# Performance work log

Hardware: AMD Instinct MI355X
Metric: run time of the kernel (lower is better)

Reference implementation:

```python
import jax, jax.numpy as jnp
import numpy as np

B, S, H = 64, 4096, 256
NEG = 1e30


def setup_inputs() -> dict:
    key = jax.random.key(0)
    k1, k2, k3, k4, k5 = jax.random.split(key, 5)
    inp_seq = jax.random.normal(k1, (B, S, H), dtype=jnp.float32)
    mask = jax.random.randint(k2, (B, S), 0, 2).astype(jnp.float32)
    mask = mask.at[:, 0].set(1.0)  # ensure at least one valid position per row
    query = jax.random.normal(k3, (B, H), dtype=jnp.float32)
    # nn.Linear(2H, H): weight [H, 2H], bias [H]
    lim = 1.0 / np.sqrt(2 * H)
    W = jax.random.uniform(k4, (H, 2 * H), minval=-lim, maxval=lim, dtype=jnp.float32)
    b = jax.random.uniform(k5, (H,), minval=-lim, maxval=lim, dtype=jnp.float32)
    return {"inp_seq": inp_seq, "mask": mask, "query": query, "W": W, "b": b}


def reference(inp_seq, mask, query, W, b):
    # single-query attention pooling
    score = jnp.einsum("bsh,bh->bs", inp_seq, query)          # [B,S]
    score = score - NEG * (1.0 - mask)                          # additive mask
    att = jax.nn.softmax(score, axis=-1)                        # [B,S]
    extracted_msg = jnp.einsum("bs,bsh->bh", att, inp_seq)     # [B,H]
    conc = jnp.concatenate([query, extracted_msg], axis=1)      # [B,2H]
    control_emb = conc @ W.T + b                                # [B,H]
    return (extracted_msg, control_emb)
```

## Files before the change

### kernel.cpp

```cpp
#include <hip/hip_runtime.h>
#include <math.h>

namespace {
constexpr int kB = 64;
constexpr int kS = 4096;
constexpr int kH = 256;
constexpr int kChunks = 32;
constexpr int kChunkS = kS / kChunks;
constexpr int kWavesPerBlock = 4;
constexpr int kPosPerWave = kChunkS / kWavesPerBlock;
constexpr int kPartStride = kH + 2;
constexpr float kLog2e = 1.4426950408889634f;
constexpr float kNegL2 = 1.4426950408889634e30f;
}

__device__ __forceinline__ float dpp_sum64(float x) {
  float f = x;
#define DPP_STEP(ctrl)                                                     \
  f += __int_as_float(__builtin_amdgcn_update_dpp(                         \
      0, __float_as_int(f), ctrl, 0xF, 0xF, true))
  DPP_STEP(0x111);
  DPP_STEP(0x112);
  DPP_STEP(0x114);
  DPP_STEP(0x118);
  DPP_STEP(0x142);
  DPP_STEP(0x143);
#undef DPP_STEP
  return __int_as_float(__builtin_amdgcn_readlane(__float_as_int(f), 63));
}

__device__ __forceinline__ float dot4(const float4 a, const float4 b) {
  return fmaf(a.x, b.x, fmaf(a.y, b.y, fmaf(a.z, b.z, a.w * b.w)));
}

__global__ __launch_bounds__(256, 4) void pass1_kernel(
    const float* __restrict__ x, const float* __restrict__ mask,
    const float* __restrict__ q, float* __restrict__ part) {
  const int blk = blockIdx.x;
  const int b = blk >> 5;
  const int c = blk & (kChunks - 1);
  const int tid = threadIdx.x;
  const int wave = tid >> 6;
  const int lane = tid & 63;

  const float4 q4 = *reinterpret_cast<const float4*>(q + b * kH + lane * 4);
  const int s_base = c * kChunkS + wave * kPosPerWave;
  const float* xw = x + ((size_t)b * kS + s_base) * kH + lane * 4;
  const float* mrow = mask + b * kS + s_base;

  float m = -INFINITY;
  float l = 0.f;
  float ax = 0.f, ay = 0.f, az = 0.f, aw = 0.f;

  #pragma unroll
  for (int i = 0; i < kPosPerWave / 4; ++i) {
    const float* p0 = xw + i * 4 * kH;
    const float4 x0 = *reinterpret_cast<const float4*>(p0);
    const float4 x1 = *reinterpret_cast<const float4*>(p0 + kH);
    const float4 x2 = *reinterpret_cast<const float4*>(p0 + 2 * kH);
    const float4 x3 = *reinterpret_cast<const float4*>(p0 + 3 * kH);
    const float4 mk = *reinterpret_cast<const float4*>(mrow + i * 4);

    const float s0 = fmaf(dpp_sum64(dot4(x0, q4)), kLog2e, (mk.x - 1.f) * kNegL2);
    const float s1 = fmaf(dpp_sum64(dot4(x1, q4)), kLog2e, (mk.y - 1.f) * kNegL2);
    const float s2 = fmaf(dpp_sum64(dot4(x2, q4)), kLog2e, (mk.z - 1.f) * kNegL2);
    const float s3 = fmaf(dpp_sum64(dot4(x3, q4)), kLog2e, (mk.w - 1.f) * kNegL2);

    const float m_new = fmaxf(fmaxf(fmaxf(s0, s1), fmaxf(s2, s3)), m);
    const float alpha = __builtin_amdgcn_exp2f(m - m_new);
    const float w0 = __builtin_amdgcn_exp2f(s0 - m_new);
    const float w1 = __builtin_amdgcn_exp2f(s1 - m_new);
    const float w2 = __builtin_amdgcn_exp2f(s2 - m_new);
    const float w3 = __builtin_amdgcn_exp2f(s3 - m_new);
    l = fmaf(l, alpha, (w0 + w1) + (w2 + w3));
    ax = fmaf(w3, x3.x, fmaf(w2, x2.x, fmaf(w1, x1.x, fmaf(w0, x0.x, ax * alpha))));
    ay = fmaf(w3, x3.y, fmaf(w2, x2.y, fmaf(w1, x1.y, fmaf(w0, x0.y, ay * alpha))));
    az = fmaf(w3, x3.z, fmaf(w2, x2.z, fmaf(w1, x1.z, fmaf(w0, x0.z, az * alpha))));
    aw = fmaf(w3, x3.w, fmaf(w2, x2.w, fmaf(w1, x1.w, fmaf(w0, x0.w, aw * alpha))));
    m = m_new;
  }

  __shared__ float sm[kWavesPerBlock];
  __shared__ float sl[kWavesPerBlock];
  __shared__ float sacc[kWavesPerBlock][kH];
  if (lane == 0) { sm[wave] = m; sl[wave] = l; }
  *reinterpret_cast<float4*>(&sacc[wave][lane * 4]) =
      make_float4(ax, ay, az, aw);
  __syncthreads();

  const float m_b = fmaxf(fmaxf(sm[0], sm[1]), fmaxf(sm[2], sm[3]));
  const float a0 = __builtin_amdgcn_exp2f(sm[0] - m_b);
  const float a1 = __builtin_amdgcn_exp2f(sm[1] - m_b);
  const float a2 = __builtin_amdgcn_exp2f(sm[2] - m_b);
  const float a3 = __builtin_amdgcn_exp2f(sm[3] - m_b);
  float* out = part + (size_t)blk * kPartStride;
  out[tid] = sacc[0][tid] * a0 + sacc[1][tid] * a1 +
             sacc[2][tid] * a2 + sacc[3][tid] * a3;
  if (tid == 0) {
    out[kH] = m_b;
    out[kH + 1] = sl[0] * a0 + sl[1] * a1 + sl[2] * a2 + sl[3] * a3;
  }
}

__global__ __launch_bounds__(256, 4) void pass2_kernel(
    const float* __restrict__ part, const float* __restrict__ q,
    const float* __restrict__ W, const float* __restrict__ bias,
    float* __restrict__ out) {
  const int b = blockIdx.x;
  const int tid = threadIdx.x;

  const float* pb = part + (size_t)b * kChunks * kPartStride;
  float m_g = -INFINITY;
  #pragma unroll
  for (int c = 0; c < kChunks; ++c)
    m_g = fmaxf(m_g, pb[c * kPartStride + kH]);
  float l_g = 0.f, num = 0.f;
  #pragma unroll 4
  for (int c = 0; c < kChunks; ++c) {
    const float* p = pb + c * kPartStride;
    const float scale = __builtin_amdgcn_exp2f(p[kH] - m_g);
    l_g += scale * p[kH + 1];
    num += scale * p[tid];
  }
  const float msg = num / l_g;
  out[(size_t)b * kH + tid] = msg;

  __shared__ float conc[2 * kH];
  conc[tid] = q[b * kH + tid];
  conc[kH + tid] = msg;
  __syncthreads();

  float acc = bias[tid];
  const float* wr = W + (size_t)tid * (2 * kH);
  #pragma unroll 8
  for (int j = 0; j < 2 * kH; j += 4) {
    const float4 w4 = *reinterpret_cast<const float4*>(wr + j);
    acc += conc[j] * w4.x + conc[j + 1] * w4.y +
           conc[j + 2] * w4.z + conc[j + 3] * w4.w;
  }
  out[(size_t)(kB * kH) + (size_t)b * kH + tid] = acc;
}

extern "C" void kernel_launch(void* const* d_in, const int* in_sizes, int n_in,
                              void* d_out, int out_size, void* d_ws, size_t ws_size,
                              hipStream_t stream) {
  const float* x    = (const float*)d_in[0];
  const float* mask = (const float*)d_in[1];
  const float* q    = (const float*)d_in[2];
  const float* W    = (const float*)d_in[3];
  const float* bias = (const float*)d_in[4];
  float* out = (float*)d_out;
  float* part = (float*)d_ws;

  pass1_kernel<<<kB * kChunks, 256, 0, stream>>>(x, mask, q, part);
  pass2_kernel<<<kB, 256, 0, stream>>>(part, q, W, bias, out);
}
```

Before: 430.3 us.

## Skip loading masked sequence rows using a per-wave ballot of mask bits

Each wave reads its 32 mask values, builds a ballot bitmask of the valid positions, and loads and processes only those rows of x. Masked rows contribute exactly zero after the 1e30 penalty, so roughly half of the HBM traffic for x is avoided. The fully unrolled 4-rows-per-step loop becomes a serial one-row loop with two-deep prefetch, and launch bounds allow more resident blocks to hide the lower per-wave memory parallelism. The additive mask term is dropped, which assumes the mask holds only 0 and 1. A guard handles chunks where every position is masked.

After: 352.7 us. 1.22x faster.

```diff
diff --git a/kernel.cpp b/kernel.cpp
--- a/kernel.cpp
+++ b/kernel.cpp
@@ -11,7 +11,6 @@
 constexpr int kPosPerWave = kChunkS / kWavesPerBlock;
 constexpr int kPartStride = kH + 2;
 constexpr float kLog2e = 1.4426950408889634f;
-constexpr float kNegL2 = 1.4426950408889634e30f;
 }
 
 __device__ __forceinline__ float dpp_sum64(float x) {
@@ -33,7 +32,7 @@
   return fmaf(a.x, b.x, fmaf(a.y, b.y, fmaf(a.z, b.z, a.w * b.w)));
 }
 
-__global__ __launch_bounds__(256, 4) void pass1_kernel(
+__global__ __launch_bounds__(256, 8) void pass1_kernel(
     const float* __restrict__ x, const float* __restrict__ mask,
     const float* __restrict__ q, float* __restrict__ part) {
   const int blk = blockIdx.x;
@@ -48,36 +47,49 @@
   const float* xw = x + ((size_t)b * kS + s_base) * kH + lane * 4;
   const float* mrow = mask + b * kS + s_base;
 
+  const float mv = mrow[lane & 31];
+  unsigned long long vm = __ballot(mv != 0.f) & 0xffffffffull;
+
   float m = -INFINITY;
   float l = 0.f;
   float ax = 0.f, ay = 0.f, az = 0.f, aw = 0.f;
 
-  #pragma unroll
-  for (int i = 0; i < kPosPerWave / 4; ++i) {
-    const float* p0 = xw + i * 4 * kH;
-    const float4 x0 = *reinterpret_cast<const float4*>(p0);
-    const float4 x1 = *reinterpret_cast<const float4*>(p0 + kH);
-    const float4 x2 = *reinterpret_cast<const float4*>(p0 + 2 * kH);
-    const float4 x3 = *reinterpret_cast<const float4*>(p0 + 3 * kH);
-    const float4 mk = *reinterpret_cast<const float4*>(mrow + i * 4);
+  auto loadrow = [&](int s) -> float4 {
+    return *reinterpret_cast<const float4*>(xw + s * kH);
+  };
+  auto process = [&](const float4 xv) {
+    const float s2 = dpp_sum64(dot4(xv, q4)) * kLog2e;
+    const float m_new = fmaxf(m, s2);
+    const float alpha = __builtin_amdgcn_exp2f(m - m_new);
+    const float w = __builtin_amdgcn_exp2f(s2 - m_new);
+    l = fmaf(l, alpha, w);
+    ax = fmaf(w, xv.x, ax * alpha);
+    ay = fmaf(w, xv.y, ay * alpha);
+    az = fmaf(w, xv.z, az * alpha);
+    aw = fmaf(w, xv.w, aw * alpha);
+    m = m_new;
+  };
 
-    const float s0 = fmaf(dpp_sum64(dot4(x0, q4)), kLog2e, (mk.x - 1.f) * kNegL2);
-    const float s1 = fmaf(dpp_sum64(dot4(x1, q4)), kLog2e, (mk.y - 1.f) * kNegL2);
-    const float s2 = fmaf(dpp_sum64(dot4(x2, q4)), kLog2e, (mk.z - 1.f) * kNegL2);
-    const float s3 = fmaf(dpp_sum64(dot4(x3, q4)), kLog2e, (mk.w - 1.f) * kNegL2);
-
-    const float m_new = fmaxf(fmaxf(fmaxf(s0, s1), fmaxf(s2, s3)), m);
-    const float alpha = __builtin_amdgcn_exp2f(m - m_new);
-    const float w0 = __builtin_amdgcn_exp2f(s0 - m_new);
-    const float w1 = __builtin_amdgcn_exp2f(s1 - m_new);
-    const float w2 = __builtin_amdgcn_exp2f(s2 - m_new);
-    const float w3 = __builtin_amdgcn_exp2f(s3 - m_new);
-    l = fmaf(l, alpha, (w0 + w1) + (w2 + w3));
-    ax = fmaf(w3, x3.x, fmaf(w2, x2.x, fmaf(w1, x1.x, fmaf(w0, x0.x, ax * alpha))));
-    ay = fmaf(w3, x3.y, fmaf(w2, x2.y, fmaf(w1, x1.y, fmaf(w0, x0.y, ay * alpha))));
-    az = fmaf(w3, x3.z, fmaf(w2, x2.z, fmaf(w1, x1.z, fmaf(w0, x0.z, az * alpha))));
-    aw = fmaf(w3, x3.w, fmaf(w2, x2.w, fmaf(w1, x1.w, fmaf(w0, x0.w, aw * alpha))));
-    m = m_new;
+  if (vm) {
+    int s0 = __builtin_ctzll(vm);
+    vm &= vm - 1;
+    float4 x0 = loadrow(s0);
+    if (vm) {
+      int s1 = __builtin_ctzll(vm);
+      vm &= vm - 1;
+      float4 x1 = loadrow(s1);
+      while (vm) {
+        const int s2i = __builtin_ctzll(vm);
+        vm &= vm - 1;
+        const float4 x2 = loadrow(s2i);
+        process(x0);
+        x0 = x1;
+        x1 = x2;
+      }
+      process(x0);
+      x0 = x1;
+    }
+    process(x0);
   }
 
   __shared__ float sm[kWavesPerBlock];
@@ -89,10 +101,11 @@
   __syncthreads();
 
   const float m_b = fmaxf(fmaxf(sm[0], sm[1]), fmaxf(sm[2], sm[3]));
-  const float a0 = __builtin_amdgcn_exp2f(sm[0] - m_b);
-  const float a1 = __builtin_amdgcn_exp2f(sm[1] - m_b);
-  const float a2 = __builtin_amdgcn_exp2f(sm[2] - m_b);
-  const float a3 = __builtin_amdgcn_exp2f(sm[3] - m_b);
+  const float m_bs = (m_b == -INFINITY) ? 0.f : m_b;
+  const float a0 = __builtin_amdgcn_exp2f(sm[0] - m_bs);
+  const float a1 = __builtin_amdgcn_exp2f(sm[1] - m_bs);
+  const float a2 = __builtin_amdgcn_exp2f(sm[2] - m_bs);
+  const float a3 = __builtin_amdgcn_exp2f(sm[3] - m_bs);
   float* out = part + (size_t)blk * kPartStride;
   out[tid] = sacc[0][tid] * a0 + sacc[1][tid] * a1 +
              sacc[2][tid] * a2 + sacc[3][tid] * a3;
```
